# Kernel tuning notes

Hardware: AMD Instinct MI355X
Metric: run time of the kernel (lower is better)

The kernel has to match this reference:

```python
import jax, jax.numpy as jnp
from jax import lax
import numpy as np

B = 512

def setup_inputs() -> dict:
    key = jax.random.key(0)
    ks = jax.random.split(key, 6)
    x = jax.random.normal(ks[0], (B, 1, 28, 28), jnp.float32)
    conv1_w = jax.random.normal(ks[1], (256, 1, 9, 9), jnp.float32) * 0.05
    conv1_b = jnp.zeros((256,), jnp.float32)
    prim_w = jax.random.normal(ks[2], (32, 32, 1, 9, 9), jnp.float32) * 0.02
    prim_b = jnp.zeros((32,), jnp.float32)
    dig_W = jax.random.normal(ks[3], (1152, 8, 16), jnp.float32) * 0.1
    dig_Wb = jnp.zeros((1152, 16), jnp.float32)
    out_w = jax.random.normal(ks[4], (10, 10, 16, 1), jnp.float32) * 0.1
    out_b = jnp.zeros((10,), jnp.float32)
    return dict(x=x, conv1_w=conv1_w, conv1_b=conv1_b, prim_w=prim_w, prim_b=prim_b,
                dig_W=dig_W, dig_Wb=dig_Wb, out_w=out_w, out_b=out_b)


def _squash(s):
    # s: [B, 16, 10]; matches torch: v = ||s||_2/(1+||s||_2) * (s^T / ||s||_1)
    l2 = jnp.sqrt(jnp.sum(s * s, axis=1))[:, :, None]      # [B, 10, 1]
    l1 = jnp.sum(jnp.abs(s), axis=1)[:, :, None]            # [B, 10, 1]
    return l2 / (1.0 + l2) * (jnp.swapaxes(s, 1, 2) / l1)   # [B, 10, 16]


def reference(x, conv1_w, conv1_b, prim_w, prim_b, dig_W, dig_Wb, out_w, out_b):
    # conv1: [B,1,28,28] -> [B,256,20,20]
    out = lax.conv_general_dilated(x, conv1_w, (1, 1), 'VALID',
                                   dimension_numbers=('NCHW', 'OIHW', 'NCHW'))
    out = jax.nn.relu(out + conv1_b[None, :, None, None])
    # primary capsules: [B,32,8,20,20] -> [B,32,8,6,6]
    out1 = out.reshape(-1, 32, 8, 20, 20)
    out1 = lax.conv_general_dilated(out1, prim_w, (1, 2, 2), 'VALID',
                                    dimension_numbers=('NCDHW', 'OIDHW', 'NCDHW'))
    out1 = jax.nn.relu(out1 + prim_b[None, :, None, None, None])
    # transpose(2,-1) then reshape -> [B, 1152, 8]
    u = jnp.swapaxes(out1, 2, 4).reshape(-1, 1152, 8)
    # per-capsule affine: [B,1152,16]
    dig = jnp.einsum('bnd,nde->bne', u, dig_W) + dig_Wb
    bsz = dig.shape[0]
    # dynamic routing: b logits are never updated in the source, so
    # c = softmax(zeros, dim=1) = 1/1152 uniform, and all 3 iterations produce
    # the identical v. Computed once (same math as the original loop).
    c = jnp.full((bsz, 1152, 10), 1.0 / 1152, dtype=dig.dtype)
    s = jnp.einsum('bni,bnd->bdi', c, dig)   # [B, 16, 10]
    v = _squash(s)                            # [B, 10, 16]
    # output Conv2d(10,10,[16,1]) on v[...,None] reduces fully -> [B,10]
    logits = jnp.einsum('bik,oik->bo', v, out_w[..., 0]) + out_b
    return jax.nn.softmax(logits, axis=1)
```

## Files before the change

kernel.cpp:

```cpp
#include <hip/hip_runtime.h>
#include <math.h>


typedef __attribute__((ext_vector_type(8))) short bf16x8;
typedef __attribute__((ext_vector_type(4))) float f32x4;

__device__ inline unsigned short f2bf(float f) {
    union { float f; unsigned u; } v; v.f = f;
    unsigned r = v.u + 0x7fff + ((v.u >> 16) & 1);
    return (unsigned short)(r >> 16);
}

#define C1TN 16008

__global__ void caps_pre(const float* __restrict__ conv1_w,
                         const float* __restrict__ prim_w,
                         const float* __restrict__ dig_Wb,
                         const float* __restrict__ out_w,
                         float* __restrict__ S,
                         float* __restrict__ colsum,
                         float* __restrict__ OW,
                         unsigned short* __restrict__ c1wp2,
                         unsigned short* __restrict__ pw2,
                         unsigned int* __restrict__ cnt,
                         int B)
{
    const int t = threadIdx.x;
    if (blockIdx.x == 468) {
        __shared__ float cs[16];
        if (t < 16) cs[t] = 0.f;
        __syncthreads();
        {
            const int k = t & 15, g = t >> 4;
            float s = 0.f;
            for (int j = 0; j < 72; ++j) s += dig_Wb[(g * 72 + j) * 16 + k];
            atomicAdd(&cs[k], s);
        }
        __syncthreads();
        if (t < 16) colsum[t] = cs[t];
        if (t >= 64 && t < 224) {
            const int idx = t - 64, o = idx >> 4, k = idx & 15;
            float s = 0.f;
            for (int i = 0; i < 10; ++i) s += out_w[(o * 10 + i) * 16 + k];
            OW[idx] = s;
        }
        return;
    }
    const int tid = blockIdx.x * 256 + t;
    if (tid < 24576) {
        const int c = tid / 96, kn = tid % 96;
        unsigned short v = 0;
        if (kn < 72) {
            const int p = kn >> 1, lo = kn & 1, ky = p >> 2, kx = 2 * (p & 3) + lo;
            v = f2bf(conv1_w[c * 81 + 9 * ky + kx]);
        } else if (kn < 81) {
            v = f2bf(conv1_w[c * 81 + 9 * (kn - 72) + 8]);
        }
        c1wp2[tid] = v;
    } else if (tid < 24576 + 87040) {
        const int j = tid - 24576;
        const int t81 = j >> 10, rem = j & 1023, o = rem >> 5, i = rem & 31;
        const int ci = (i >> 1) + ((i & 1) << 4);
        pw2[j] = (t81 < 81) ? f2bf(prim_w[(o * 32 + ci) * 81 + t81]) : (unsigned short)0;
    } else {
        const int k = tid - 111616;
        if (k < B * 16) {
            S[k] = 0.f;
            if (k < B) cnt[k] = 0u;
        }
    }
}

__global__ __launch_bounds__(256, 4) void caps_main(
    const float* __restrict__ x,
    const float* __restrict__ conv1_b,
    const float* __restrict__ prim_b,
    const float* __restrict__ dig_W,
    const unsigned short* __restrict__ c1wp2,
    const unsigned short* __restrict__ pw2,
    float* __restrict__ S,
    const float* __restrict__ colsum,
    const float* __restrict__ OW,
    const float* __restrict__ out_b,
    unsigned int* __restrict__ cnt,
    float* __restrict__ out)
{
    __shared__ __align__(16) unsigned short c1t[C1TN];
    __shared__ __align__(16) unsigned imgp[1344];
    __shared__ unsigned short offT[64];
    __shared__ float pbs[32];
    __shared__ float sacc[64];

    const int b = blockIdx.x >> 3, d = blockIdx.x & 7;
    const int t = threadIdx.x;
    const int wave = t >> 6, lane = t & 63, quad = lane >> 4, l16 = lane & 15;

    const float* xb = x + b * 784;
    for (int j = t; j < 1344; j += 256) {
        unsigned v = 0;
        if (j < 784) {
            const float a = xb[j];
            const int xc = j - 28 * (int)(((unsigned)j * 37450u) >> 20);
            const float c = (xc < 27) ? xb[j + 1] : 0.f;
            v = (unsigned)f2bf(a) | ((unsigned)f2bf(c) << 16);
        }
        imgp[j] = v;
    }
    if (t < 64) {
        int v;
        if (t < 32) {
            const int ky = t >> 2, kx = 2 * (t & 3);
            v = ky * 28 + kx;
        } else {
            const int k = t + 32;
            if (k < 72) {
                const int p = k >> 1, lo = k & 1, ky = p >> 2, kx = 2 * (p & 3) + lo;
                v = ky * 28 + kx;
            } else if (k < 81) {
                v = (k - 72) * 28 + 8;
            } else v = 784;
        }
        offT[t] = (unsigned short)(4 * v);
    }
    if (t < 32) pbs[t] = prim_b[t];
    __syncthreads();

    unsigned tp0[4], tp1[4], t2a[4], t2b[4];
#pragma unroll
    for (int r = 0; r < 4; ++r) {
        tp0[r] = offT[quad * 4 + r];
        tp1[r] = offT[16 + quad * 4 + r];
        t2a[r] = offT[32 + quad * 8 + 2 * r];
        t2b[r] = offT[32 + quad * 8 + 2 * r + 1];
    }

    {
        const float cb0 = conv1_b[l16 * 8 + d];
        const float cb1 = conv1_b[(16 + l16) * 8 + d];
        bf16x8 Bw0[3], Bw1[3];
#pragma unroll
        for (int ks = 0; ks < 3; ++ks) {
            Bw0[ks] = *(const bf16x8*)&c1wp2[(l16 * 8 + d) * 96 + ks * 32 + quad * 8];
            Bw1[ks] = *(const bf16x8*)&c1wp2[((16 + l16) * 8 + d) * 96 + ks * 32 + quad * 8];
        }
        for (int mt = wave; mt < 25; mt += 4) {
            const int pos = mt * 16 + l16;
            const int y = (int)(((unsigned)pos * 52429u) >> 20);
            const unsigned pb4 = (unsigned)(pos + 8 * y) * 4u;
            f32x4 a0 = {0.f, 0.f, 0.f, 0.f}, a1 = {0.f, 0.f, 0.f, 0.f};
            union { unsigned u[4]; bf16x8 v; } A;
#pragma unroll
            for (int r = 0; r < 4; ++r)
                A.u[r] = *(const unsigned*)((const char*)imgp + (pb4 + tp0[r]));
            a0 = __builtin_amdgcn_mfma_f32_16x16x32_bf16(A.v, Bw0[0], a0, 0, 0, 0);
            a1 = __builtin_amdgcn_mfma_f32_16x16x32_bf16(A.v, Bw1[0], a1, 0, 0, 0);
#pragma unroll
            for (int r = 0; r < 4; ++r)
                A.u[r] = *(const unsigned*)((const char*)imgp + (pb4 + tp1[r]));
            a0 = __builtin_amdgcn_mfma_f32_16x16x32_bf16(A.v, Bw0[1], a0, 0, 0, 0);
            a1 = __builtin_amdgcn_mfma_f32_16x16x32_bf16(A.v, Bw1[1], a1, 0, 0, 0);
#pragma unroll
            for (int r = 0; r < 4; ++r) {
                const unsigned lo = *(const unsigned*)((const char*)imgp + (pb4 + t2a[r]));
                const unsigned hi = *(const unsigned*)((const char*)imgp + (pb4 + t2b[r]));
                A.u[r] = (lo & 0xFFFFu) | (hi << 16);
            }
            a0 = __builtin_amdgcn_mfma_f32_16x16x32_bf16(A.v, Bw0[2], a0, 0, 0, 0);
            a1 = __builtin_amdgcn_mfma_f32_16x16x32_bf16(A.v, Bw1[2], a1, 0, 0, 0);
#pragma unroll
            for (int r = 0; r < 4; ++r) {
                const int pr = mt * 16 + quad * 4 + r;
                const int spar = (int)((((unsigned)pr * 52429u) >> 21) & 1u);
                const int base = pr * 40 + 8 * spar;
                const unsigned pk = (unsigned)f2bf(fmaxf(a0[r] + cb0, 0.f))
                                  | ((unsigned)f2bf(fmaxf(a1[r] + cb1, 0.f)) << 16);
                *(unsigned*)&c1t[base + 2 * l16] = pk;
            }
        }
    }
    __syncthreads();

    const int hp = l16 >> 3, wp = l16 & 7;
    const unsigned Lbase = 80u * (unsigned)(40 * hp + 2 * wp) + 16u * quad;
    const unsigned Lh0 = Lbase + 16u * hp;
    const unsigned Lh1 = Lbase + 16u * (1 - hp);

    f32x4 pa[6];
#pragma unroll
    for (int q = 0; q < 6; ++q) pa[q] = (f32x4){0.f, 0.f, 0.f, 0.f};

    {
        const unsigned short* apbase = pw2 + l16 * 32 + quad * 8;
        int off = wave;
        bf16x8 A0 = *(const bf16x8*)(apbase + off * 1024);
        bf16x8 A1 = *(const bf16x8*)(apbase + off * 1024 + 512);
        for (; off < 81; off += 4) {
            const int noff = off + 4;
            const bf16x8 nA0 = *(const bf16x8*)(apbase + noff * 1024);
            const bf16x8 nA1 = *(const bf16x8*)(apbase + noff * 1024 + 512);
            const int ky = (off * 57) >> 9;
            const int kx = off - 9 * ky;
            const int kk = (ky >> 1) & 1;
            const unsigned soff = 80u * (unsigned)(20 * ky + kx);
            const unsigned ad = (kk ? Lh1 : Lh0) + soff;
            const char* b0 = (const char*)c1t + ad;
#pragma unroll
            for (int nt = 0; nt < 3; ++nt) {
                const bf16x8 Bf = *(const bf16x8*)(b0 + nt * 6400);
                pa[nt]     = __builtin_amdgcn_mfma_f32_16x16x32_bf16(A0, Bf, pa[nt],     0, 0, 0);
                pa[3 + nt] = __builtin_amdgcn_mfma_f32_16x16x32_bf16(A1, Bf, pa[3 + nt], 0, 0, 0);
            }
            A0 = nA0; A1 = nA1;
        }
    }
    __syncthreads();

    f32x4* redbuf = (f32x4*)c1t;
#pragma unroll
    for (int q = 0; q < 6; ++q) redbuf[(wave * 6 + q) * 64 + lane] = pa[q];
    __syncthreads();

    float part[16];
#pragma unroll
    for (int k = 0; k < 16; ++k) part[k] = 0.f;

#define FOLDQ(QV)                                                           \
    {                                                                       \
        const int q = (QV);                                                 \
        f32x4 u4 = redbuf[q * 64 + lane];                                   \
        u4 += redbuf[(6 + q) * 64 + lane];                                  \
        u4 += redbuf[(12 + q) * 64 + lane];                                 \
        u4 += redbuf[(18 + q) * 64 + lane];                                 \
        if (wp < 6) {                                                       \
            const int mt = (q >= 3) ? 1 : 0;                                \
            const int nt = q - 3 * mt;                                      \
            const int h = 2 * nt + hp;                                      \
            _Pragma("unroll")                                               \
            for (int r = 0; r < 4; ++r) {                                   \
                const int o = mt * 16 + quad * 4 + r;                       \
                const float val = fmaxf(u4[r] + pbs[o], 0.f);               \
                const int nc = o * 36 + wp * 6 + h;                         \
                const f32x4* wd = (const f32x4*)&dig_W[(nc * 8 + d) * 16];  \
                _Pragma("unroll")                                           \
                for (int m = 0; m < 4; ++m) {                               \
                    const f32x4 wv = wd[m];                                 \
                    part[m * 4 + 0] = fmaf(val, wv[0], part[m * 4 + 0]);    \
                    part[m * 4 + 1] = fmaf(val, wv[1], part[m * 4 + 1]);    \
                    part[m * 4 + 2] = fmaf(val, wv[2], part[m * 4 + 2]);    \
                    part[m * 4 + 3] = fmaf(val, wv[3], part[m * 4 + 3]);    \
                }                                                           \
            }                                                               \
        }                                                                   \
    }

    FOLDQ(wave);
    if (wave < 2) FOLDQ(wave + 4);
#undef FOLDQ

#pragma unroll
    for (int k = 0; k < 16; ++k) {
        float v = part[k];
        v += __shfl_xor(v, 32, 64);
        v += __shfl_xor(v, 16, 64);
        v += __shfl_xor(v, 8, 64);
        v += __shfl_xor(v, 4, 64);
        v += __shfl_xor(v, 2, 64);
        v += __shfl_xor(v, 1, 64);
        part[k] = v;
    }
    if (lane == 0) {
#pragma unroll
        for (int k = 0; k < 16; ++k) sacc[wave * 16 + k] = part[k];
    }
    __syncthreads();
    if (t < 16) {
        const float v = sacc[t] + sacc[16 + t] + sacc[32 + t] + sacc[48 + t];
        atomicAdd(&S[b * 16 + t], v);
    }
    __syncthreads();

    if (t == 0) {
        const unsigned old = atomicAdd(&cnt[b], 1u);
        if (old == 7u) {
            float Sv[16]; float l2 = 0.f, l1 = 0.f;
#pragma unroll
            for (int k = 0; k < 16; ++k) {
                const float sv = (__hip_atomic_load(&S[b * 16 + k], __ATOMIC_RELAXED,
                                                    __HIP_MEMORY_SCOPE_AGENT)
                                  + colsum[k]) * (1.f / 1152.f);
                Sv[k] = sv; l2 += sv * sv; l1 += fabsf(sv);
            }
            l2 = sqrtf(l2);
            const float sc = l2 / (1.f + l2) / l1;
            float lg[10]; float mx = -1e30f;
#pragma unroll
            for (int o = 0; o < 10; ++o) {
                float a = out_b[o];
#pragma unroll
                for (int k = 0; k < 16; ++k) a = fmaf(Sv[k] * sc, OW[o * 16 + k], a);
                lg[o] = a; mx = fmaxf(mx, a);
            }
            float sum = 0.f;
#pragma unroll
            for (int o = 0; o < 10; ++o) { lg[o] = expf(lg[o] - mx); sum += lg[o]; }
            const float inv = 1.f / sum;
#pragma unroll
            for (int o = 0; o < 10; ++o) out[b * 10 + o] = lg[o] * inv;
        }
    }
}

extern "C" void kernel_launch(void* const* d_in, const int* in_sizes, int n_in,
                              void* d_out, int out_size, void* d_ws, size_t ws_size,
                              hipStream_t stream) {
    const float* x       = (const float*)d_in[0];
    const float* conv1_w = (const float*)d_in[1];
    const float* conv1_b = (const float*)d_in[2];
    const float* prim_w  = (const float*)d_in[3];
    const float* prim_b  = (const float*)d_in[4];
    const float* dig_W   = (const float*)d_in[5];
    const float* dig_Wb  = (const float*)d_in[6];
    const float* out_w   = (const float*)d_in[7];
    const float* out_b   = (const float*)d_in[8];
    float* out = (float*)d_out;

    const int B = in_sizes[0] / 784;

    char* w = (char*)d_ws;
    float* S              = (float*)(w);
    float* colsum         = (float*)(w + 32768);
    float* OW             = (float*)(w + 32832);
    unsigned short* c1wp2 = (unsigned short*)(w + 33472);
    unsigned short* pw2   = (unsigned short*)(w + 33472 + 49152);
    unsigned int* cnt     = (unsigned int*)(w + 33472 + 49152 + 174080);

    caps_pre<<<469, 256, 0, stream>>>(conv1_w, prim_w, dig_Wb, out_w,
                                      S, colsum, OW, c1wp2, pw2, cnt, B);
    caps_main<<<B * 8, 256, 0, stream>>>(x, conv1_b, prim_b, dig_W, c1wp2, pw2,
                                         S, colsum, OW, out_b, cnt, out);
}
```

Before: 174.2 us.

## Coalesce prim weight repack via LDS, hoist A loads, use halving wave reduction

The prim_w repack now runs one block per output channel: each block stages the channel's weights in shared memory so the global reads are coalesced, replacing scattered strided reads. The first A-fragment loads in caps_main are hoisted to kernel entry so they overlap the image staging and conv1 phase. The 16-value wave reduction becomes a recursive-halving exchange that issues far fewer shuffles. Each change is small, and caps_pre is a minor share of total time.

```diff
diff --git a/kernel.cpp b/kernel.cpp
--- a/kernel.cpp
+++ b/kernel.cpp
@@ -26,7 +26,37 @@
                          int B)
 {
     const int t = threadIdx.x;
-    if (blockIdx.x == 468) {
+    const int bx = blockIdx.x;
+
+    if (bx < 32) {
+        __shared__ float lw[2592];
+        const float* src = prim_w + bx * 32 * 81;
+        for (int j = t; j < 2592; j += 256) lw[j] = src[j];
+        __syncthreads();
+        unsigned short* dst = pw2 + bx * 32;
+        for (int f = t; f < 2720; f += 256) {
+            const int tap = f >> 5, s = f & 31;
+            const int ci = (s >> 1) + ((s & 1) << 4);
+            const unsigned short v =
+                (tap < 81) ? f2bf(lw[ci * 81 + tap]) : (unsigned short)0;
+            dst[tap * 1024 + s] = v;
+        }
+        return;
+    }
+    if (bx < 128) {
+        const int tid = (bx - 32) * 256 + t;
+        const int c = tid / 96, kn = tid % 96;
+        unsigned short v = 0;
+        if (kn < 72) {
+            const int p = kn >> 1, lo = kn & 1, ky = p >> 2, kx = 2 * (p & 3) + lo;
+            v = f2bf(conv1_w[c * 81 + 9 * ky + kx]);
+        } else if (kn < 81) {
+            v = f2bf(conv1_w[c * 81 + 9 * (kn - 72) + 8]);
+        }
+        c1wp2[tid] = v;
+        return;
+    }
+    if (bx == 128) {
         __shared__ float cs[16];
         if (t < 16) cs[t] = 0.f;
         __syncthreads();
@@ -46,29 +76,9 @@
         }
         return;
     }
-    const int tid = blockIdx.x * 256 + t;
-    if (tid < 24576) {
-        const int c = tid / 96, kn = tid % 96;
-        unsigned short v = 0;
-        if (kn < 72) {
-            const int p = kn >> 1, lo = kn & 1, ky = p >> 2, kx = 2 * (p & 3) + lo;
-            v = f2bf(conv1_w[c * 81 + 9 * ky + kx]);
-        } else if (kn < 81) {
-            v = f2bf(conv1_w[c * 81 + 9 * (kn - 72) + 8]);
-        }
-        c1wp2[tid] = v;
-    } else if (tid < 24576 + 87040) {
-        const int j = tid - 24576;
-        const int t81 = j >> 10, rem = j & 1023, o = rem >> 5, i = rem & 31;
-        const int ci = (i >> 1) + ((i & 1) << 4);
-        pw2[j] = (t81 < 81) ? f2bf(prim_w[(o * 32 + ci) * 81 + t81]) : (unsigned short)0;
-    } else {
-        const int k = tid - 111616;
-        if (k < B * 16) {
-            S[k] = 0.f;
-            if (k < B) cnt[k] = 0u;
-        }
-    }
+    const int idx = (bx - 129) * 256 + t;
+    if (idx < B * 16) S[idx] = 0.f;
+    else if (idx < B * 17) cnt[idx - B * 16] = 0u;
 }
 
 __global__ __launch_bounds__(256, 4) void caps_main(
@@ -95,6 +105,10 @@
     const int t = threadIdx.x;
     const int wave = t >> 6, lane = t & 63, quad = lane >> 4, l16 = lane & 15;
 
+    const unsigned short* apbase = pw2 + l16 * 32 + quad * 8;
+    bf16x8 A0 = *(const bf16x8*)(apbase + wave * 1024);
+    bf16x8 A1 = *(const bf16x8*)(apbase + wave * 1024 + 512);
+
     const float* xb = x + b * 784;
     for (int j = t; j < 1344; j += 256) {
         unsigned v = 0;
@@ -190,10 +204,7 @@
     for (int q = 0; q < 6; ++q) pa[q] = (f32x4){0.f, 0.f, 0.f, 0.f};
 
     {
-        const unsigned short* apbase = pw2 + l16 * 32 + quad * 8;
         int off = wave;
-        bf16x8 A0 = *(const bf16x8*)(apbase + off * 1024);
-        bf16x8 A1 = *(const bf16x8*)(apbase + off * 1024 + 512);
         for (; off < 81; off += 4) {
             const int noff = off + 4;
             const bf16x8 nA0 = *(const bf16x8*)(apbase + noff * 1024);
@@ -257,21 +268,46 @@
     if (wave < 2) FOLDQ(wave + 4);
 #undef FOLDQ
 
-#pragma unroll
-    for (int k = 0; k < 16; ++k) {
-        float v = part[k];
-        v += __shfl_xor(v, 32, 64);
-        v += __shfl_xor(v, 16, 64);
-        v += __shfl_xor(v, 8, 64);
-        v += __shfl_xor(v, 4, 64);
-        v += __shfl_xor(v, 2, 64);
-        v += __shfl_xor(v, 1, 64);
-        part[k] = v;
-    }
-    if (lane == 0) {
-#pragma unroll
-        for (int k = 0; k < 16; ++k) sacc[wave * 16 + k] = part[k];
-    }
+    float v8[8];
+    {
+        const bool hi5 = (lane & 32) != 0;
+#pragma unroll
+        for (int j = 0; j < 8; ++j) {
+            const float keep = hi5 ? part[8 + j] : part[j];
+            const float send = hi5 ? part[j] : part[8 + j];
+            v8[j] = keep + __shfl_xor(send, 32, 64);
+        }
+    }
+    float v4[4];
+    {
+        const bool hi4 = (lane & 16) != 0;
+#pragma unroll
+        for (int j = 0; j < 4; ++j) {
+            const float keep = hi4 ? v8[4 + j] : v8[j];
+            const float send = hi4 ? v8[j] : v8[4 + j];
+            v4[j] = keep + __shfl_xor(send, 16, 64);
+        }
+    }
+    float v2[2];
+    {
+        const bool hi3 = (lane & 8) != 0;
+#pragma unroll
+        for (int j = 0; j < 2; ++j) {
+            const float keep = hi3 ? v4[2 + j] : v4[j];
+            const float send = hi3 ? v4[j] : v4[2 + j];
+            v2[j] = keep + __shfl_xor(send, 8, 64);
+        }
+    }
+    float v1;
+    {
+        const bool hi2 = (lane & 4) != 0;
+        const float keep = hi2 ? v2[1] : v2[0];
+        const float send = hi2 ? v2[0] : v2[1];
+        v1 = keep + __shfl_xor(send, 4, 64);
+    }
+    v1 += __shfl_xor(v1, 2, 64);
+    v1 += __shfl_xor(v1, 1, 64);
+    if ((lane & 3) == 0) sacc[wave * 16 + ((lane >> 2) & 15)] = v1;
     __syncthreads();
     if (t < 16) {
         const float v = sacc[t] + sacc[16 + t] + sacc[32 + t] + sacc[48 + t];
@@ -334,8 +370,9 @@
     unsigned short* pw2   = (unsigned short*)(w + 33472 + 49152);
     unsigned int* cnt     = (unsigned int*)(w + 33472 + 49152 + 174080);
 
-    caps_pre<<<469, 256, 0, stream>>>(conv1_w, prim_w, dig_Wb, out_w,
-                                      S, colsum, OW, c1wp2, pw2, cnt, B);
+    const int zblocks = (B * 17 + 255) / 256;
+    caps_pre<<<129 + zblocks, 256, 0, stream>>>(conv1_w, prim_w, dig_Wb, out_w,
+                                                S, colsum, OW, c1wp2, pw2, cnt, B);
     caps_main<<<B * 8, 256, 0, stream>>>(x, conv1_b, prim_b, dig_W, c1wp2, pw2,
                                          S, colsum, OW, out_b, cnt, out);
 }
```

After: 176.1 us. No clear change (+1.1%).
